# Kernel tuning notes

Hardware: AMD Instinct MI355X
Metric: run time of the kernel (lower is better)

The kernel has to match this reference:

```python
import jax, jax.numpy as jnp
import numpy as np
import math

DIM = 1024
MAX_SEQ_LEN = 8192

def setup_inputs() -> dict:
    key = jax.random.key(0)
    k1, k2, k3, k4 = jax.random.split(key, 4)
    x = jax.random.normal(k1, (4, 4096, DIM), dtype=jnp.float32)
    base_phases = jax.random.normal(k2, (MAX_SEQ_LEN, DIM), dtype=jnp.float32) * math.pi
    # nn.Linear(dim, dim): weight [out, in], bias [out]
    bound = 1.0 / math.sqrt(DIM)
    W = jax.random.uniform(k3, (DIM, DIM), dtype=jnp.float32, minval=-bound, maxval=bound)
    b = jax.random.uniform(k4, (DIM,), dtype=jnp.float32, minval=-bound, maxval=bound)
    return {"x": x, "base_phases": base_phases, "W": W, "b": b}

def reference(x, base_phases, W, b):
    B, L, D = x.shape
    phases = base_phases[:L][None, :, :]          # [1, L, D]
    value = jnp.einsum('bld,ed->ble', x, W) + b   # Linear: x @ W.T + b
    cos_p = jnp.cos(phases)
    sin_p = jnp.sin(phases)
    mem_real = jnp.cumsum(value * cos_p, axis=1)
    mem_imag = jnp.cumsum(value * sin_p, axis=1)
    retrieved = mem_real * cos_p + mem_imag * sin_p
    positions = jnp.arange(1, L + 1, dtype=jnp.float32)
    norm = jnp.sqrt(positions)[None, :, None]     # [1, L, 1]
    return retrieved / norm
```

## Files before the change

### kernel.cpp

```cpp
#include <hip/hip_runtime.h>
#include <hip/hip_bf16.h>

#define DIM 1024
#define SEQ 4096
#define NB 4
#define MROWS (NB * SEQ)
#define NC 64
#define CL (SEQ / NC)

#define BM 256
#define BN 256
#define BK 32
#define NT (DIM / BK)
#define TILE_LDS 32768
#define GEMM_LDS (4 * TILE_LDS)

typedef __attribute__((ext_vector_type(8))) short bf16x8;
typedef __attribute__((ext_vector_type(4))) float f32x4;

static __device__ __forceinline__ unsigned short f2bf(float f) {
    union { float f; unsigned u; } v; v.f = f;
    unsigned r = v.u + 0x7FFF + ((v.u >> 16) & 1);
    return (unsigned short)(r >> 16);
}

static __device__ __forceinline__ float bf2f(unsigned short h) {
    union { unsigned u; float f; } v; v.u = ((unsigned)h) << 16;
    return v.f;
}

static __device__ __forceinline__ void gload_lds16(const void* g, void* l) {
    __builtin_amdgcn_global_load_lds((const __attribute__((address_space(1))) void*)g,
                                     (__attribute__((address_space(3))) void*)l, 16, 0, 0);
}

__global__ void convert_kernel(const float* __restrict__ x, const float* __restrict__ W,
                               unsigned short* __restrict__ xb, unsigned short* __restrict__ wb) {
    const long long NX4 = (long long)MROWS * DIM / 4;
    const long long NW4 = (long long)DIM * DIM / 4;
    long long t = (long long)blockIdx.x * blockDim.x + threadIdx.x;
    if (t < NX4) {
        float4 v = ((const float4*)x)[t];
        ushort4 o;
        o.x = f2bf(v.x); o.y = f2bf(v.y); o.z = f2bf(v.z); o.w = f2bf(v.w);
        ((ushort4*)xb)[t] = o;
    } else if (t < NX4 + NW4) {
        long long u = t - NX4;
        float4 v = ((const float4*)W)[u];
        ushort4 o;
        o.x = f2bf(v.x); o.y = f2bf(v.y); o.z = f2bf(v.z); o.w = f2bf(v.w);
        ((ushort4*)wb)[u] = o;
    }
}

static __device__ __forceinline__ void stage_A(const unsigned short* __restrict__ A, char* smem,
                                               int q, int m0, int ks, int w, int lane) {
#pragma unroll
    for (int r = 0; r < 2; ++r) {
        int row  = r * 128 + w * 16 + (lane >> 2);
        int c16  = (lane & 3) ^ (row & 3);
        const unsigned short* g = A + (size_t)(m0 + row) * DIM + ks + c16 * 8;
        char* l = smem + q * TILE_LDS + (r * 128 + w * 16) * 64 + lane * 16;
        gload_lds16(g, l);
    }
}

static __device__ __forceinline__ void stage_B(const unsigned short* __restrict__ Bm, char* smem,
                                               int q, int n0, int ks, int w, int lane) {
#pragma unroll
    for (int r = 0; r < 2; ++r) {
        int row  = r * 128 + w * 16 + (lane >> 2);
        int c16  = (lane & 3) ^ (row & 3);
        const unsigned short* g = Bm + (size_t)(n0 + row) * DIM + ks + c16 * 8;
        char* l = smem + q * TILE_LDS + 16384 + (r * 128 + w * 16) * 64 + lane * 16;
        gload_lds16(g, l);
    }
}

__global__ __launch_bounds__(512, 2) void gemm_kernel(const unsigned short* __restrict__ A,
                                                      const unsigned short* __restrict__ Bm,
                                                      const float* __restrict__ bias,
                                                      unsigned short* __restrict__ V) {
    extern __shared__ char smem[];
    const int tid  = threadIdx.x;
    const int lane = tid & 63;
    const int w    = tid >> 6;
    const int wm   = w >> 2;
    const int wn   = w & 3;
    const int wr   = wm * 128;
    const int wc   = wn * 64;
    const int rl   = lane & 15;
    const int rh   = lane >> 4;
    const int swz  = ((rh ^ (rl & 3)) * 16);
    const int m0   = blockIdx.x * BM;
    const int n0   = blockIdx.y * BN;

    f32x4 acc[8][4];
#pragma unroll
    for (int m = 0; m < 8; ++m)
#pragma unroll
        for (int n = 0; n < 4; ++n)
            acc[m][n] = (f32x4){0.f, 0.f, 0.f, 0.f};

#pragma unroll
    for (int s = 0; s < 3; ++s) {
        stage_A(A, smem, s, m0, s * BK, w, lane);
        stage_B(Bm, smem, s, n0, s * BK, w, lane);
    }

#pragma unroll 4
    for (int t = 0; t < NT; ++t) {
        const int q = t & 3;
        asm volatile("s_waitcnt vmcnt(8)" ::: "memory");
        __builtin_amdgcn_s_barrier();

        const int snext = t + 3;
        const int qn = snext & 3;
        const int ksn = (snext & (NT - 1)) * BK;
        char* base = smem + q * TILE_LDS;

        bf16x8 bfr[4];
#pragma unroll
        for (int nf = 0; nf < 4; ++nf)
            bfr[nf] = *(const bf16x8*)(base + 16384 + (wc + nf * 16 + rl) * 64 + swz);
        bf16x8 af[4];
#pragma unroll
        for (int mf = 0; mf < 4; ++mf)
            af[mf] = *(const bf16x8*)(base + (wr + mf * 16 + rl) * 64 + swz);
        stage_A(A, smem, qn, m0, ksn, w, lane);
        __builtin_amdgcn_s_setprio(1);
#pragma unroll
        for (int mf = 0; mf < 4; ++mf)
#pragma unroll
            for (int nf = 0; nf < 4; ++nf)
                acc[mf][nf] = __builtin_amdgcn_mfma_f32_16x16x32_bf16(af[mf], bfr[nf], acc[mf][nf], 0, 0, 0);
        __builtin_amdgcn_s_setprio(0);

#pragma unroll
        for (int mf = 0; mf < 4; ++mf)
            af[mf] = *(const bf16x8*)(base + (wr + (mf + 4) * 16 + rl) * 64 + swz);
        stage_B(Bm, smem, qn, n0, ksn, w, lane);
        __builtin_amdgcn_s_setprio(1);
#pragma unroll
        for (int mf = 0; mf < 4; ++mf)
#pragma unroll
            for (int nf = 0; nf < 4; ++nf)
                acc[mf + 4][nf] = __builtin_amdgcn_mfma_f32_16x16x32_bf16(af[mf], bfr[nf], acc[mf + 4][nf], 0, 0, 0);
        __builtin_amdgcn_s_setprio(0);
    }

#pragma unroll
    for (int mf = 0; mf < 8; ++mf) {
#pragma unroll
        for (int nf = 0; nf < 4; ++nf) {
            int gcol = n0 + wc + nf * 16 + rl;
            float bv = bias[gcol];
#pragma unroll
            for (int j = 0; j < 4; ++j) {
                int grow = m0 + wr + mf * 16 + rh * 4 + j;
                V[(size_t)grow * DIM + gcol] = f2bf(acc[mf][nf][j] + bv);
            }
        }
    }
}

__global__ void passA_kernel(const unsigned short* __restrict__ val, const float* __restrict__ ph,
                             float* __restrict__ pr, float* __restrict__ pi) {
    int t  = blockIdx.x * 256 + threadIdx.x;
    int c  = blockIdx.y;
    int bb = blockIdx.z;
    const ushort2* v = (const ushort2*)val + ((size_t)bb * SEQ + (size_t)c * CL) * (DIM / 2) + t;
    const float2*  p = (const float2*)ph + (size_t)c * CL * (DIM / 2) + t;
    float sr0 = 0.f, si0 = 0.f, sr1 = 0.f, si1 = 0.f;
    for (int l = 0; l < CL; ++l) {
        ushort2 vv = v[(size_t)l * (DIM / 2)];
        float2  pp = p[(size_t)l * (DIM / 2)];
        float v0 = bf2f(vv.x), v1 = bf2f(vv.y);
        float s0, c0, s1, c1;
        __sincosf(pp.x, &s0, &c0);
        __sincosf(pp.y, &s1, &c1);
        sr0 += v0 * c0; si0 += v0 * s0;
        sr1 += v1 * c1; si1 += v1 * s1;
    }
    size_t idx = ((size_t)bb * NC + c) * DIM + 2 * t;
    pr[idx] = sr0; pr[idx + 1] = sr1;
    pi[idx] = si0; pi[idx + 1] = si1;
}

__global__ void passB_kernel(float* __restrict__ pr, float* __restrict__ pi) {
    int t = blockIdx.x * 256 + threadIdx.x;
    int bb = t >> 10;
    int e  = t & 1023;
    float r = 0.f, im = 0.f;
    for (int c = 0; c < NC; ++c) {
        size_t idx = ((size_t)bb * NC + c) * DIM + e;
        float tr = pr[idx], ti = pi[idx];
        pr[idx] = r; pi[idx] = im;
        r += tr; im += ti;
    }
}

__global__ void passC_kernel(const unsigned short* __restrict__ val, const float* __restrict__ ph,
                             const float* __restrict__ pr, const float* __restrict__ pi,
                             float* __restrict__ out) {
    int t  = blockIdx.x * 256 + threadIdx.x;
    int c  = blockIdx.y;
    int bb = blockIdx.z;
    size_t base = ((size_t)bb * SEQ + (size_t)c * CL) * (DIM / 2) + t;
    const ushort2* v = (const ushort2*)val + base;
    const float2*  p = (const float2*)ph + (size_t)c * CL * (DIM / 2) + t;
    float2* o = (float2*)out + base;
    size_t pidx = ((size_t)bb * NC + c) * DIM + 2 * t;
    float ar0 = pr[pidx], ar1 = pr[pidx + 1];
    float ai0 = pi[pidx], ai1 = pi[pidx + 1];
    const int l0 = c * CL;
    for (int l = 0; l < CL; ++l) {
        ushort2 vv = v[(size_t)l * (DIM / 2)];
        float2  pp = p[(size_t)l * (DIM / 2)];
        float v0 = bf2f(vv.x), v1 = bf2f(vv.y);
        float s0, c0, s1, c1;
        __sincosf(pp.x, &s0, &c0);
        __sincosf(pp.y, &s1, &c1);
        ar0 += v0 * c0; ai0 += v0 * s0;
        ar1 += v1 * c1; ai1 += v1 * s1;
        float rn = rsqrtf((float)(l0 + l + 1));
        float2 ov;
        ov.x = (ar0 * c0 + ai0 * s0) * rn;
        ov.y = (ar1 * c1 + ai1 * s1) * rn;
        o[(size_t)l * (DIM / 2)] = ov;
    }
}

extern "C" void kernel_launch(void* const* d_in, const int* in_sizes, int n_in,
                              void* d_out, int out_size, void* d_ws, size_t ws_size,
                              hipStream_t stream) {
    const float* x  = (const float*)d_in[0];
    const float* ph = (const float*)d_in[1];
    const float* W  = (const float*)d_in[2];
    const float* b  = (const float*)d_in[3];
    float* out = (float*)d_out;

    unsigned short* xb = (unsigned short*)d_out;
    unsigned short* wb = xb + (size_t)MROWS * DIM;

    unsigned short* vb = (unsigned short*)d_ws;
    float* pr = (float*)(vb + (size_t)MROWS * DIM);
    float* pi = pr + (size_t)NB * NC * DIM;

    (void)hipFuncSetAttribute((const void*)gemm_kernel,
                              hipFuncAttributeMaxDynamicSharedMemorySize, GEMM_LDS);

    {
        long long total4 = (long long)MROWS * DIM / 4 + (long long)DIM * DIM / 4;
        int blocks = (int)((total4 + 255) / 256);
        convert_kernel<<<blocks, 256, 0, stream>>>(x, W, xb, wb);
    }
    {
        dim3 grid(MROWS / BM, DIM / BN);
        gemm_kernel<<<grid, 512, GEMM_LDS, stream>>>(xb, wb, b, vb);
    }
    {
        dim3 grid(DIM / 512, NC, NB);
        passA_kernel<<<grid, 256, 0, stream>>>(vb, ph, pr, pi);
    }
    passB_kernel<<<16, 256, 0, stream>>>(pr, pi);
    {
        dim3 grid(DIM / 512, NC, NB);
        passC_kernel<<<grid, 256, 0, stream>>>(vb, ph, pr, pi, out);
    }
}
```

Before: 93.69 us.

## Restructure GEMM main loop with ping-pong barriers and new LDS swizzle

Changes the LDS XOR swizzle to depend on row bits 1-2 instead of 0-1, intended to remove bank conflicts on the fragment reads. Replaces the single per-iteration wait/barrier with several workgroup barriers and sched_barriers around each MFMA cluster, so waves alternate between memory and compute phases in lockstep. Also hoists the bias loads out of the epilogue. The extra barriers add synchronisation cost and may reduce overlap if the waves do not interleave well.

New measurement: 93.76 us. About the same (+0.1%).

```diff
diff --git a/kernel.cpp b/kernel.cpp
--- a/kernel.cpp
+++ b/kernel.cpp
@@ -55,10 +55,10 @@
 
 static __device__ __forceinline__ void stage_A(const unsigned short* __restrict__ A, char* smem,
                                                int q, int m0, int ks, int w, int lane) {
+    const int c16 = (lane & 3) ^ ((lane >> 3) & 3);
 #pragma unroll
     for (int r = 0; r < 2; ++r) {
-        int row  = r * 128 + w * 16 + (lane >> 2);
-        int c16  = (lane & 3) ^ (row & 3);
+        int row = r * 128 + w * 16 + (lane >> 2);
         const unsigned short* g = A + (size_t)(m0 + row) * DIM + ks + c16 * 8;
         char* l = smem + q * TILE_LDS + (r * 128 + w * 16) * 64 + lane * 16;
         gload_lds16(g, l);
@@ -67,10 +67,10 @@
 
 static __device__ __forceinline__ void stage_B(const unsigned short* __restrict__ Bm, char* smem,
                                                int q, int n0, int ks, int w, int lane) {
+    const int c16 = (lane & 3) ^ ((lane >> 3) & 3);
 #pragma unroll
     for (int r = 0; r < 2; ++r) {
-        int row  = r * 128 + w * 16 + (lane >> 2);
-        int c16  = (lane & 3) ^ (row & 3);
+        int row = r * 128 + w * 16 + (lane >> 2);
         const unsigned short* g = Bm + (size_t)(n0 + row) * DIM + ks + c16 * 8;
         char* l = smem + q * TILE_LDS + 16384 + (r * 128 + w * 16) * 64 + lane * 16;
         gload_lds16(g, l);
@@ -91,7 +91,7 @@
     const int wc   = wn * 64;
     const int rl   = lane & 15;
     const int rh   = lane >> 4;
-    const int swz  = ((rh ^ (rl & 3)) * 16);
+    const int swz  = (rh ^ ((rl >> 1) & 3)) * 16;
     const int m0   = blockIdx.x * BM;
     const int n0   = blockIdx.y * BN;
 
@@ -101,22 +101,25 @@
 #pragma unroll
         for (int n = 0; n < 4; ++n)
             acc[m][n] = (f32x4){0.f, 0.f, 0.f, 0.f};
+
+    float bv[4];
+#pragma unroll
+    for (int nf = 0; nf < 4; ++nf)
+        bv[nf] = bias[n0 + wc + nf * 16 + rl];
 
 #pragma unroll
     for (int s = 0; s < 3; ++s) {
         stage_A(A, smem, s, m0, s * BK, w, lane);
         stage_B(Bm, smem, s, n0, s * BK, w, lane);
     }
+    asm volatile("s_waitcnt vmcnt(8)" ::: "memory");
+    __builtin_amdgcn_s_barrier();
 
 #pragma unroll 4
     for (int t = 0; t < NT; ++t) {
-        const int q = t & 3;
-        asm volatile("s_waitcnt vmcnt(8)" ::: "memory");
-        __builtin_amdgcn_s_barrier();
-
-        const int snext = t + 3;
-        const int qn = snext & 3;
-        const int ksn = (snext & (NT - 1)) * BK;
+        const int q  = t & 3;
+        const int qn = (t + 3) & 3;
+        const int ksn = ((t + 3) & (NT - 1)) * BK;
         char* base = smem + q * TILE_LDS;
 
         bf16x8 bfr[4];
@@ -128,6 +131,10 @@
         for (int mf = 0; mf < 4; ++mf)
             af[mf] = *(const bf16x8*)(base + (wr + mf * 16 + rl) * 64 + swz);
         stage_A(A, smem, qn, m0, ksn, w, lane);
+        __builtin_amdgcn_sched_barrier(0);
+        __builtin_amdgcn_s_barrier();
+        asm volatile("s_waitcnt lgkmcnt(0)" ::: "memory");
+        __builtin_amdgcn_sched_barrier(0);
         __builtin_amdgcn_s_setprio(1);
 #pragma unroll
         for (int mf = 0; mf < 4; ++mf)
@@ -135,11 +142,18 @@
             for (int nf = 0; nf < 4; ++nf)
                 acc[mf][nf] = __builtin_amdgcn_mfma_f32_16x16x32_bf16(af[mf], bfr[nf], acc[mf][nf], 0, 0, 0);
         __builtin_amdgcn_s_setprio(0);
+        __builtin_amdgcn_sched_barrier(0);
+        __builtin_amdgcn_s_barrier();
 
 #pragma unroll
         for (int mf = 0; mf < 4; ++mf)
             af[mf] = *(const bf16x8*)(base + (wr + (mf + 4) * 16 + rl) * 64 + swz);
         stage_B(Bm, smem, qn, n0, ksn, w, lane);
+        asm volatile("s_waitcnt vmcnt(8)" ::: "memory");
+        __builtin_amdgcn_sched_barrier(0);
+        __builtin_amdgcn_s_barrier();
+        asm volatile("s_waitcnt lgkmcnt(0)" ::: "memory");
+        __builtin_amdgcn_sched_barrier(0);
         __builtin_amdgcn_s_setprio(1);
 #pragma unroll
         for (int mf = 0; mf < 4; ++mf)
@@ -147,6 +161,8 @@
             for (int nf = 0; nf < 4; ++nf)
                 acc[mf + 4][nf] = __builtin_amdgcn_mfma_f32_16x16x32_bf16(af[mf], bfr[nf], acc[mf + 4][nf], 0, 0, 0);
         __builtin_amdgcn_s_setprio(0);
+        __builtin_amdgcn_sched_barrier(0);
+        __builtin_amdgcn_s_barrier();
     }
 
 #pragma unroll
@@ -154,11 +170,10 @@
 #pragma unroll
         for (int nf = 0; nf < 4; ++nf) {
             int gcol = n0 + wc + nf * 16 + rl;
-            float bv = bias[gcol];
 #pragma unroll
             for (int j = 0; j < 4; ++j) {
                 int grow = m0 + wr + mf * 16 + rh * 4 + j;
-                V[(size_t)grow * DIM + gcol] = f2bf(acc[mf][nf][j] + bv);
+                V[(size_t)grow * DIM + gcol] = f2bf(acc[mf][nf][j] + bv[nf]);
             }
         }
     }
```

## Shrink GEMM N-tile to 128 with 3-slot LDS ring and vectorized epilogue

Applied to the files above, without the earlier changes.

The bf16 GEMM now uses 256x128 tiles instead of 256x256, with three LDS slots instead of four, allowing four blocks per CU instead of two. The MFMA operands are swapped so each lane holds four consecutive output columns, which lets the epilogue write 8-byte vector stores with preloaded float4 bias rather than scalar 2-byte stores. The swizzle pattern and the wait count are adjusted to match the new layout. Smaller tiles lower the arithmetic intensity per block and double the number of A-tile loads, in exchange for better occupancy and coalesced stores.

Result: slower. 102.5 us (+9.4%).

```diff
diff --git a/kernel.cpp b/kernel.cpp
--- a/kernel.cpp
+++ b/kernel.cpp
@@ -9,11 +9,11 @@
 #define CL (SEQ / NC)
 
 #define BM 256
-#define BN 256
+#define BN 128
 #define BK 32
-#define NT (DIM / BK)
-#define TILE_LDS 32768
-#define GEMM_LDS (4 * TILE_LDS)
+#define NTK 32
+#define SLOTB 24576
+#define GEMM_LDS (3 * SLOTB)
 
 typedef __attribute__((ext_vector_type(8))) short bf16x8;
 typedef __attribute__((ext_vector_type(4))) float f32x4;
@@ -53,31 +53,29 @@
     }
 }
 
+
 static __device__ __forceinline__ void stage_A(const unsigned short* __restrict__ A, char* smem,
-                                               int q, int m0, int ks, int w, int lane) {
+                                               int slot, int m0, int ks, int w, int lane) {
+    const int c16 = (lane & 3) ^ ((lane >> 3) & 3);
 #pragma unroll
     for (int r = 0; r < 2; ++r) {
-        int row  = r * 128 + w * 16 + (lane >> 2);
-        int c16  = (lane & 3) ^ (row & 3);
+        int row = r * 128 + w * 16 + (lane >> 2);
         const unsigned short* g = A + (size_t)(m0 + row) * DIM + ks + c16 * 8;
-        char* l = smem + q * TILE_LDS + (r * 128 + w * 16) * 64 + lane * 16;
+        char* l = smem + (size_t)slot * SLOTB + (r * 128 + w * 16) * 64 + lane * 16;
         gload_lds16(g, l);
     }
 }
 
 static __device__ __forceinline__ void stage_B(const unsigned short* __restrict__ Bm, char* smem,
-                                               int q, int n0, int ks, int w, int lane) {
-#pragma unroll
-    for (int r = 0; r < 2; ++r) {
-        int row  = r * 128 + w * 16 + (lane >> 2);
-        int c16  = (lane & 3) ^ (row & 3);
-        const unsigned short* g = Bm + (size_t)(n0 + row) * DIM + ks + c16 * 8;
-        char* l = smem + q * TILE_LDS + 16384 + (r * 128 + w * 16) * 64 + lane * 16;
-        gload_lds16(g, l);
-    }
-}
-
-__global__ __launch_bounds__(512, 2) void gemm_kernel(const unsigned short* __restrict__ A,
+                                               int slot, int n0, int ks, int w, int lane) {
+    const int c16 = (lane & 3) ^ ((lane >> 3) & 3);
+    int row = w * 16 + (lane >> 2);
+    const unsigned short* g = Bm + (size_t)(n0 + row) * DIM + ks + c16 * 8;
+    char* l = smem + (size_t)slot * SLOTB + 16384 + (w * 16) * 64 + lane * 16;
+    gload_lds16(g, l);
+}
+
+__global__ __launch_bounds__(512, 4) void gemm_kernel(const unsigned short* __restrict__ A,
                                                       const unsigned short* __restrict__ Bm,
                                                       const float* __restrict__ bias,
                                                       unsigned short* __restrict__ V) {
@@ -85,81 +83,82 @@
     const int tid  = threadIdx.x;
     const int lane = tid & 63;
     const int w    = tid >> 6;
-    const int wm   = w >> 2;
-    const int wn   = w & 3;
-    const int wr   = wm * 128;
-    const int wc   = wn * 64;
+    const int wr   = (w >> 2) * 128;
+    const int wc   = (w & 3) * 32;
     const int rl   = lane & 15;
     const int rh   = lane >> 4;
-    const int swz  = ((rh ^ (rl & 3)) * 16);
+    const int swz  = (rh ^ ((rl >> 1) & 3)) * 16;
     const int m0   = blockIdx.x * BM;
     const int n0   = blockIdx.y * BN;
 
-    f32x4 acc[8][4];
+    f32x4 acc[8][2];
 #pragma unroll
     for (int m = 0; m < 8; ++m)
 #pragma unroll
-        for (int n = 0; n < 4; ++n)
+        for (int n = 0; n < 2; ++n)
             acc[m][n] = (f32x4){0.f, 0.f, 0.f, 0.f};
 
-#pragma unroll
-    for (int s = 0; s < 3; ++s) {
-        stage_A(A, smem, s, m0, s * BK, w, lane);
-        stage_B(Bm, smem, s, n0, s * BK, w, lane);
-    }
-
-#pragma unroll 4
-    for (int t = 0; t < NT; ++t) {
-        const int q = t & 3;
-        asm volatile("s_waitcnt vmcnt(8)" ::: "memory");
+    float4 bv4[2];
+#pragma unroll
+    for (int nf = 0; nf < 2; ++nf)
+        bv4[nf] = *(const float4*)(bias + n0 + wc + nf * 16 + rh * 4);
+
+    stage_A(A, smem, 0, m0, 0, w, lane);
+    stage_B(Bm, smem, 0, n0, 0, w, lane);
+    stage_A(A, smem, 1, m0, BK, w, lane);
+    stage_B(Bm, smem, 1, n0, BK, w, lane);
+
+#pragma unroll 1
+    for (int t = 0; t < NTK; ++t) {
+        asm volatile("s_waitcnt vmcnt(3)" ::: "memory");
         __builtin_amdgcn_s_barrier();
-
-        const int snext = t + 3;
-        const int qn = snext & 3;
-        const int ksn = (snext & (NT - 1)) * BK;
-        char* base = smem + q * TILE_LDS;
-
-        bf16x8 bfr[4];
-#pragma unroll
-        for (int nf = 0; nf < 4; ++nf)
-            bfr[nf] = *(const bf16x8*)(base + 16384 + (wc + nf * 16 + rl) * 64 + swz);
+        const int sc = t % 3;
+        const int ss = (t + 2) % 3;
+        const int kn = ((t + 2) & (NTK - 1)) * BK;
+        const char* sb = smem + (size_t)sc * SLOTB;
+
+        bf16x8 bfr[2];
+#pragma unroll
+        for (int nf = 0; nf < 2; ++nf)
+            bfr[nf] = *(const bf16x8*)(sb + 16384 + (wc + nf * 16 + rl) * 64 + swz);
         bf16x8 af[4];
 #pragma unroll
         for (int mf = 0; mf < 4; ++mf)
-            af[mf] = *(const bf16x8*)(base + (wr + mf * 16 + rl) * 64 + swz);
-        stage_A(A, smem, qn, m0, ksn, w, lane);
+            af[mf] = *(const bf16x8*)(sb + (wr + mf * 16 + rl) * 64 + swz);
+        stage_A(A, smem, ss, m0, kn, w, lane);
         __builtin_amdgcn_s_setprio(1);
 #pragma unroll
         for (int mf = 0; mf < 4; ++mf)
 #pragma unroll
-            for (int nf = 0; nf < 4; ++nf)
-                acc[mf][nf] = __builtin_amdgcn_mfma_f32_16x16x32_bf16(af[mf], bfr[nf], acc[mf][nf], 0, 0, 0);
+            for (int nf = 0; nf < 2; ++nf)
+                acc[mf][nf] = __builtin_amdgcn_mfma_f32_16x16x32_bf16(bfr[nf], af[mf], acc[mf][nf], 0, 0, 0);
         __builtin_amdgcn_s_setprio(0);
 
 #pragma unroll
         for (int mf = 0; mf < 4; ++mf)
-            af[mf] = *(const bf16x8*)(base + (wr + (mf + 4) * 16 + rl) * 64 + swz);
-        stage_B(Bm, smem, qn, n0, ksn, w, lane);
+            af[mf] = *(const bf16x8*)(sb + (wr + (mf + 4) * 16 + rl) * 64 + swz);
+        stage_B(Bm, smem, ss, n0, kn, w, lane);
         __builtin_amdgcn_s_setprio(1);
 #pragma unroll
         for (int mf = 0; mf < 4; ++mf)
 #pragma unroll
-            for (int nf = 0; nf < 4; ++nf)
-                acc[mf + 4][nf] = __builtin_amdgcn_mfma_f32_16x16x32_bf16(af[mf], bfr[nf], acc[mf + 4][nf], 0, 0, 0);
+            for (int nf = 0; nf < 2; ++nf)
+                acc[mf + 4][nf] = __builtin_amdgcn_mfma_f32_16x16x32_bf16(bfr[nf], af[mf], acc[mf + 4][nf], 0, 0, 0);
         __builtin_amdgcn_s_setprio(0);
     }
 
 #pragma unroll
     for (int mf = 0; mf < 8; ++mf) {
-#pragma unroll
-        for (int nf = 0; nf < 4; ++nf) {
-            int gcol = n0 + wc + nf * 16 + rl;
-            float bv = bias[gcol];
-#pragma unroll
-            for (int j = 0; j < 4; ++j) {
-                int grow = m0 + wr + mf * 16 + rh * 4 + j;
-                V[(size_t)grow * DIM + gcol] = f2bf(acc[mf][nf][j] + bv);
-            }
+        int grow = m0 + wr + mf * 16 + rl;
+#pragma unroll
+        for (int nf = 0; nf < 2; ++nf) {
+            int gcol0 = n0 + wc + nf * 16 + rh * 4;
+            ushort4 o;
+            o.x = f2bf(acc[mf][nf][0] + bv4[nf].x);
+            o.y = f2bf(acc[mf][nf][1] + bv4[nf].y);
+            o.z = f2bf(acc[mf][nf][2] + bv4[nf].z);
+            o.w = f2bf(acc[mf][nf][3] + bv4[nf].w);
+            *(ushort4*)(V + (size_t)grow * DIM + gcol0) = o;
         }
     }
 }
```
